# Performance work log

Measured on AMD Instinct MI355X. Metric: run time of the kernel, lower is better.

The kernel has to match this reference:

```python
import jax, jax.numpy as jnp
import numpy as np

B, S, D = 2, 2048, 1024
H, DK = 16, 64
DFF = 4096
WINDOW = 128
GLOBAL = 16
EPS = 1e-5


def _layer_norm(x, g, b):
    mu = jnp.mean(x, axis=-1, keepdims=True)
    var = jnp.var(x, axis=-1, keepdims=True)
    return (x - mu) * jax.lax.rsqrt(var + EPS) * g + b


def setup_inputs() -> dict:
    key = jax.random.key(0)
    ks = jax.random.split(key, 12)
    s = 0.02
    inp = {
        "x": jax.random.normal(ks[0], (B, S, D), dtype=jnp.float32),
        "Wq": jax.random.normal(ks[1], (D, D), jnp.float32) * s,
        "bq": jnp.zeros((D,), jnp.float32),
        "Wk": jax.random.normal(ks[2], (D, D), jnp.float32) * s,
        "bk": jnp.zeros((D,), jnp.float32),
        "Wv": jax.random.normal(ks[3], (D, D), jnp.float32) * s,
        "bv": jnp.zeros((D,), jnp.float32),
        "Wo": jax.random.normal(ks[4], (D, D), jnp.float32) * s,
        "bo": jnp.zeros((D,), jnp.float32),
        "ln1_g": jnp.ones((D,), jnp.float32),
        "ln1_b": jnp.zeros((D,), jnp.float32),
        "W1": jax.random.normal(ks[5], (D, DFF), jnp.float32) * s,
        "b1": jnp.zeros((DFF,), jnp.float32),
        "W2": jax.random.normal(ks[6], (DFF, D), jnp.float32) * s,
        "b2": jnp.zeros((D,), jnp.float32),
        "ln2_g": jnp.ones((D,), jnp.float32),
        "ln2_b": jnp.zeros((D,), jnp.float32),
    }
    return inp


def _local_global_mask(seq_len):
    # token i attends to j iff |i-j| <= WINDOW, or i < GLOBAL, or j < GLOBAL
    i = jnp.arange(seq_len)[:, None]
    j = jnp.arange(seq_len)[None, :]
    m = jnp.abs(i - j) <= WINDOW
    m = m | (i < GLOBAL) | (j < GLOBAL)
    return m  # [S, S] bool


def reference(x, Wq, bq, Wk, bk, Wv, bv, Wo, bo, ln1_g, ln1_b,
              W1, b1, W2, b2, ln2_g, ln2_b):
    # --- self-attention sublayer (pre-norm residual) ---
    xn = _layer_norm(x, ln1_g, ln1_b)
    q = (xn @ Wq + bq).reshape(B, S, H, DK).transpose(0, 2, 1, 3)  # [B,H,S,DK]
    k = (xn @ Wk + bk).reshape(B, S, H, DK).transpose(0, 2, 1, 3)
    v = (xn @ Wv + bv).reshape(B, S, H, DK).transpose(0, 2, 1, 3)

    scores = jnp.einsum('bhqd,bhkd->bhqk', q, k) / jnp.sqrt(jnp.float32(DK))
    mask = _local_global_mask(S)  # [S,S]
    scores = jnp.where(mask[None, None], scores, jnp.float32(-jnp.inf))
    attn = jax.nn.softmax(scores, axis=-1)
    out = jnp.einsum('bhqk,bhkd->bhqd', attn, v)
    out = out.transpose(0, 2, 1, 3).reshape(B, S, D)
    out = out @ Wo + bo
    x = x + out

    # --- feed-forward sublayer (pre-norm residual) ---
    xn2 = _layer_norm(x, ln2_g, ln2_b)
    h = jax.nn.gelu(xn2 @ W1 + b1, approximate=False)
    ff = h @ W2 + b2
    x = x + ff
    return x
```

## Files before the change

### kernel.cpp

```cpp
#include <hip/hip_runtime.h>
#include <stdint.h>


typedef unsigned short u16;
typedef unsigned int   u32;
typedef __attribute__((ext_vector_type(8))) short  short8;
typedef __attribute__((ext_vector_type(4))) float  f32x4;

#define S_LEN   2048
#define D_MODEL 1024
#define ROWS    4096

__device__ __forceinline__ float bf2f(u16 u) {
  union { u32 i; float f; } v; v.i = ((u32)u) << 16; return v.f;
}
__device__ __forceinline__ float bflo(u32 u) {
  union { u32 i; float f; } v; v.i = u << 16; return v.f;
}
__device__ __forceinline__ float bfhi(u32 u) {
  union { u32 i; float f; } v; v.i = u & 0xffff0000u; return v.f;
}
__device__ __forceinline__ u16 f2bf(float f) {
  union { float f; u32 i; } v; v.f = f;
  u32 r = v.i + 0x7fffu + ((v.i >> 16) & 1u);
  return (u16)(r >> 16);
}

__device__ __forceinline__ void gld_lds16(const u16* g, u16* l) {
  __attribute__((address_space(3))) u32* lp =
      reinterpret_cast<__attribute__((address_space(3))) u32*>(
          reinterpret_cast<uintptr_t>(l));
  const __attribute__((address_space(1))) u32* gp =
      reinterpret_cast<const __attribute__((address_space(1))) u32*>(
          reinterpret_cast<uintptr_t>(g));
  __builtin_amdgcn_global_load_lds(gp, lp, 16, 0, 0);
}


#define GBAR  __builtin_amdgcn_s_barrier()
#define LGKM0 asm volatile("s_waitcnt lgkmcnt(0)" ::: "memory")
#define VM4   asm volatile("s_waitcnt vmcnt(4)" ::: "memory")
#define VM0   asm volatile("s_waitcnt vmcnt(0)" ::: "memory")

#define STAGE_A(buf, t, hm) do {                                              \
    gld_lds16(pA[hm][0] + (size_t)(t) * 64, &Ald[buf][0][(hm)*4096 + ldst]);  \
    gld_lds16(pA[hm][1] + (size_t)(t) * 64, &Ald[buf][1][(hm)*4096 + ldst]);  \
  } while (0)

#define STAGE_B(buf, t, hm) do {                                              \
    gld_lds16(pB[hm][0] + (size_t)(t) * 64, &Bld[buf][0][(hm)*4096 + ldst]);  \
    gld_lds16(pB[hm][1] + (size_t)(t) * 64, &Bld[buf][1][(hm)*4096 + ldst]);  \
  } while (0)

#define READ_B(buf) do {                                                      \
    _Pragma("unroll") for (int nj = 0; nj < 4; ++nj) {                        \
      bfv[nj][0] = *(const short8*)&Bld[buf][0][brow + nj * 512];             \
      bfv[nj][1] = *(const short8*)&Bld[buf][1][brow + nj * 512]; }           \
  } while (0)

#define READ_A(buf, q) do {                                                   \
    af[0][0] = *(const short8*)&Ald[buf][0][arow + (2*(q)) * 512];            \
    af[0][1] = *(const short8*)&Ald[buf][1][arow + (2*(q)) * 512];            \
    af[1][0] = *(const short8*)&Ald[buf][0][arow + (2*(q)+1) * 512];          \
    af[1][1] = *(const short8*)&Ald[buf][1][arow + (2*(q)+1) * 512];          \
  } while (0)

#define MFMA_Q(q) do {                                                        \
    __builtin_amdgcn_s_setprio(1);                                            \
    _Pragma("unroll") for (int dm = 0; dm < 2; ++dm)                          \
    _Pragma("unroll") for (int kk = 0; kk < 2; ++kk)                          \
    _Pragma("unroll") for (int nj = 0; nj < 4; ++nj)                          \
      acc[2*(q)+dm][nj] = __builtin_amdgcn_mfma_f32_16x16x32_bf16(            \
          af[dm][kk], bfv[nj][kk], acc[2*(q)+dm][nj], 0, 0, 0);               \
    __builtin_amdgcn_s_setprio(0);                                            \
  } while (0)

#define PHASE(buf, q, STAGE_STMT, TAILWAIT) do {                              \
    if ((q) == 0) READ_B(buf);                                                \
    READ_A(buf, q);                                                           \
    STAGE_STMT;                                                               \
    GBAR;                                                                     \
    LGKM0;                                                                    \
    MFMA_Q(q);                                                                \
    TAILWAIT;                                                                 \
    GBAR;                                                                     \
  } while (0)

template <int EPI>
__global__ __launch_bounds__(512) void gemm256(
    const u16* __restrict__ A, const u16* __restrict__ Bt,
    const float* __restrict__ bias, u16* __restrict__ C,
    int N, int K)
{
  __shared__ __attribute__((aligned(16))) u16 Ald[2][2][256 * 32];
  __shared__ __attribute__((aligned(16))) u16 Bld[2][2][256 * 32];

  const int tid  = threadIdx.x;
  const int w    = tid >> 6;
  const int lane = tid & 63;
  const int wm   = w >> 2;
  const int wn   = w & 3;
  const int lm   = lane & 15;
  const int kq   = lane >> 4;
  const int bm   = blockIdx.y * 256;
  const int bn   = blockIdx.x * 256;

  const int rslot = ((kq + (lm >> 1)) & 3) * 8;
  const int arow  = (wm * 128 + lm) * 32 + rslot;
  const int brow  = (wn * 64  + lm) * 32 + rslot;

  const int gcoff = (((lane & 3) - (lane >> 3)) & 3) * 8;
  const int srow  = w * 16 + (lane >> 2);
  const int ldst  = w * 512;

  const u16* pA[2][2];
  const u16* pB[2][2];
#pragma unroll
  for (int hm = 0; hm < 2; ++hm)
#pragma unroll
    for (int j = 0; j < 2; ++j) {
      pA[hm][j] = A  + (size_t)(bm + hm * 128 + srow) * K + j * 32 + gcoff;
      pB[hm][j] = Bt + (size_t)(bn + hm * 128 + srow) * K + j * 32 + gcoff;
    }

  f32x4 acc[8][4];
#pragma unroll
  for (int i = 0; i < 8; ++i)
#pragma unroll
    for (int j = 0; j < 4; ++j) acc[i][j] = (f32x4){0.f, 0.f, 0.f, 0.f};

  short8 af[2][2];
  short8 bfv[4][2];

  const int P = K >> 7;

  STAGE_B(0, 0, 0); STAGE_B(0, 0, 1);
  STAGE_A(0, 0, 0); STAGE_A(0, 0, 1);
  STAGE_B(1, 1, 0); STAGE_B(1, 1, 1);
  VM4;
  GBAR;

  for (int i = 0; i < P - 1; ++i) {
    const int t1 = 2 * i + 1, t2 = 2 * i + 2, t3 = 2 * i + 3;
    PHASE(0, 0, STAGE_A(1, t1, 0), );
    PHASE(0, 1, STAGE_A(1, t1, 1), );
    PHASE(0, 2, STAGE_B(0, t2, 0), );
    PHASE(0, 3, STAGE_B(0, t2, 1), VM4);
    PHASE(1, 0, STAGE_A(0, t2, 0), );
    PHASE(1, 1, STAGE_A(0, t2, 1), );
    PHASE(1, 2, STAGE_B(1, t3, 0), );
    PHASE(1, 3, STAGE_B(1, t3, 1), VM4);
  }
  {
    const int t1 = 2 * P - 1;
    PHASE(0, 0, STAGE_A(1, t1, 0), );
    PHASE(0, 1, STAGE_A(1, t1, 1), );
    PHASE(0, 2, , );
    PHASE(0, 3, , VM0);
    PHASE(1, 0, , );
    PHASE(1, 1, , );
    PHASE(1, 2, , );
    PHASE(1, 3, , );
  }

  const int r0 = kq * 4;
#pragma unroll
  for (int mi = 0; mi < 8; ++mi) {
#pragma unroll
    for (int r = 0; r < 4; ++r) {
      const int grow = bm + wm * 128 + mi * 16 + r0 + r;
#pragma unroll
      for (int nj = 0; nj < 4; ++nj) {
        const int gcol = bn + wn * 64 + nj * 16 + lm;
        float v = acc[mi][nj][r] + bias[gcol];
        if (EPI == 1) v = 0.5f * v * (1.0f + erff(v * 0.70710678118654752f));
        C[(size_t)grow * N + gcol] = f2bf(v);
      }
    }
  }
}

__global__ __launch_bounds__(256) void gemm_sp(
    const u16* __restrict__ A, const u16* __restrict__ Bt,
    u16* __restrict__ P0, u16* __restrict__ P1,
    int M, int N, int K, int KH)
{
  __shared__ __attribute__((aligned(16))) u16 As[2][128 * 32];
  __shared__ __attribute__((aligned(16))) u16 Bs[2][128 * 32];
  const int tid  = threadIdx.x;
  const int wave = tid >> 6;
  const int lane = tid & 63;
  const int bm = blockIdx.y * 128;
  const int bn = blockIdx.x * 128;
  const int kz = blockIdx.z;
  u16* P = kz ? P1 : P0;
  const int wr = (wave >> 1) * 64;
  const int wc = (wave & 1) * 64;
  const int lm = lane & 15;
  const int kq = lane >> 4;

  f32x4 acc[4][4];
#pragma unroll
  for (int i = 0; i < 4; ++i)
#pragma unroll
    for (int j = 0; j < 4; ++j) acc[i][j] = (f32x4){0.f, 0.f, 0.f, 0.f};

  const int srow = wave * 16 + (lane >> 2);
  const int kg   = (((lane & 3) - (srow >> 1)) & 3) * 8;
  const u16* gA = A  + (size_t)(bm + srow) * K + kz * KH + kg;
  const u16* gB = Bt + (size_t)(bn + srow) * K + kz * KH + kg;
  const int wb = (wave * 16) * 32;

  gld_lds16(gA, &As[0][wb]);
  gld_lds16(gA + (size_t)64 * K, &As[0][wb + 64 * 32]);
  gld_lds16(gB, &Bs[0][wb]);
  gld_lds16(gB + (size_t)64 * K, &Bs[0][wb + 64 * 32]);

  int buf = 0;
  for (int k0 = 0; k0 < KH; k0 += 32, buf ^= 1) {
    __syncthreads();
    const int kn = k0 + 32;
    if (kn < KH) {
      gld_lds16(gA + kn, &As[buf ^ 1][wb]);
      gld_lds16(gA + (size_t)64 * K + kn, &As[buf ^ 1][wb + 64 * 32]);
      gld_lds16(gB + kn, &Bs[buf ^ 1][wb]);
      gld_lds16(gB + (size_t)64 * K + kn, &Bs[buf ^ 1][wb + 64 * 32]);
    }

    short8 af[4], bfv[4];
#pragma unroll
    for (int ti = 0; ti < 4; ++ti) {
      const int Ra = wr + ti * 16 + lm;
      af[ti] = *(const short8*)&As[buf][Ra * 32 + (((kq + (Ra >> 1)) & 3) * 8)];
    }
#pragma unroll
    for (int tj = 0; tj < 4; ++tj) {
      const int Rb = wc + tj * 16 + lm;
      bfv[tj] = *(const short8*)&Bs[buf][Rb * 32 + (((kq + (Rb >> 1)) & 3) * 8)];
    }
#pragma unroll
    for (int ti = 0; ti < 4; ++ti)
#pragma unroll
      for (int tj = 0; tj < 4; ++tj)
        acc[ti][tj] = __builtin_amdgcn_mfma_f32_16x16x32_bf16(
            af[ti], bfv[tj], acc[ti][tj], 0, 0, 0);
  }

  const int r0 = (lane >> 4) * 4;
#pragma unroll
  for (int ti = 0; ti < 4; ++ti) {
#pragma unroll
    for (int r = 0; r < 4; ++r) {
      const int grow = bm + wr + ti * 16 + r0 + r;
#pragma unroll
      for (int tj = 0; tj < 4; ++tj) {
        const int gcol = bn + wc + tj * 16 + lm;
        P[(size_t)grow * N + gcol] = f2bf(acc[ti][tj][r]);
      }
    }
  }
}

__global__ __launch_bounds__(256) void reduce2(
    const u16* __restrict__ P0, const u16* __restrict__ P1,
    const float* __restrict__ bias, const float* res, float* out)
{
  const size_t base = ((size_t)blockIdx.x * 256 + threadIdx.x) * 8;
  const int col = (int)(base & 1023);
  uint4 p0 = *(const uint4*)(P0 + base);
  uint4 p1 = *(const uint4*)(P1 + base);
  float4 b0 = *(const float4*)(bias + col);
  float4 b1 = *(const float4*)(bias + col + 4);
  float4 r0 = *(const float4*)(res + base);
  float4 r1 = *(const float4*)(res + base + 4);
  float4 o0, o1;
  o0.x = bflo(p0.x) + bflo(p1.x) + b0.x + r0.x;
  o0.y = bfhi(p0.x) + bfhi(p1.x) + b0.y + r0.y;
  o0.z = bflo(p0.y) + bflo(p1.y) + b0.z + r0.z;
  o0.w = bfhi(p0.y) + bfhi(p1.y) + b0.w + r0.w;
  o1.x = bflo(p0.z) + bflo(p1.z) + b1.x + r1.x;
  o1.y = bfhi(p0.z) + bfhi(p1.z) + b1.y + r1.y;
  o1.z = bflo(p0.w) + bflo(p1.w) + b1.z + r1.z;
  o1.w = bfhi(p0.w) + bfhi(p1.w) + b1.w + r1.w;
  *(float4*)(out + base) = o0;
  *(float4*)(out + base + 4) = o1;
}

__global__ __launch_bounds__(256) void ln_kernel(
    const float* __restrict__ x, const float* __restrict__ g,
    const float* __restrict__ b, u16* __restrict__ o)
{
  const int row = blockIdx.x;
  const int t = threadIdx.x;
  float4 v = *(const float4*)(x + (size_t)row * D_MODEL + t * 4);
  float s  = v.x + v.y + v.z + v.w;
  float ss = v.x * v.x + v.y * v.y + v.z * v.z + v.w * v.w;
#pragma unroll
  for (int off = 32; off > 0; off >>= 1) {
    s  += __shfl_down(s, off);
    ss += __shfl_down(ss, off);
  }
  __shared__ float sm[4], ssm[4], stat[2];
  if ((t & 63) == 0) { sm[t >> 6] = s; ssm[t >> 6] = ss; }
  __syncthreads();
  if (t == 0) {
    float S = sm[0] + sm[1] + sm[2] + sm[3];
    float SS = ssm[0] + ssm[1] + ssm[2] + ssm[3];
    float mu = S * (1.0f / 1024.0f);
    float var = SS * (1.0f / 1024.0f) - mu * mu;
    stat[0] = mu;
    stat[1] = rsqrtf(fmaxf(var, 0.0f) + 1e-5f);
  }
  __syncthreads();
  const float mu = stat[0], rstd = stat[1];
  float4 gg = *(const float4*)(g + t * 4);
  float4 bb = *(const float4*)(b + t * 4);
  u16 o0 = f2bf((v.x - mu) * rstd * gg.x + bb.x);
  u16 o1 = f2bf((v.y - mu) * rstd * gg.y + bb.y);
  u16 o2 = f2bf((v.z - mu) * rstd * gg.z + bb.z);
  u16 o3 = f2bf((v.w - mu) * rstd * gg.w + bb.w);
  uint2 w;
  w.x = (u32)o0 | ((u32)o1 << 16);
  w.y = (u32)o2 | ((u32)o3 << 16);
  *(uint2*)(o + (size_t)row * D_MODEL + t * 4) = w;
}

__global__ __launch_bounds__(256) void attn_band(
    const u16* __restrict__ qkv, u16* __restrict__ out)
{
  const int t    = threadIdx.x;
  const int w    = t >> 6;
  const int lane = t & 63;
  const int m    = lane & 15;
  const int quad = lane >> 4;
  const int bh   = blockIdx.y;
  const int b    = bh >> 4, h = bh & 15;
  const int i0   = blockIdx.x * 64;
  const size_t bb = (size_t)b * S_LEN;

  __shared__ __attribute__((aligned(16))) u16 Ks[32 * 72];
  __shared__ __attribute__((aligned(16))) u16 Vt[64 * 40];
  __shared__ __attribute__((aligned(16))) u16 Ps[4][16 * 40];

  const u16* qrow = qkv + (bb + i0 + 16 * w + m) * 3072 + h * 64;
  const short8 aq0 = *(const short8*)(qrow + quad * 8);
  const short8 aq1 = *(const short8*)(qrow + 32 + quad * 8);

  f32x4 Ov[4];
#pragma unroll
  for (int td = 0; td < 4; ++td) Ov[td] = (f32x4){0.f, 0.f, 0.f, 0.f};
  float mP[4] = {-1e30f, -1e30f, -1e30f, -1e30f};
  float lS[4] = {0.f, 0.f, 0.f, 0.f};

  const int iB = i0 + 16 * w + quad * 4;

  const int lo = max(32, i0 - 128);
  const int hi = min(S_LEN, i0 + 192);
  const int nChunks = 1 + (hi - lo) / 32;

  const int skr = t >> 3;
  const int skc = (t & 7) * 8;

  for (int c = 0; c < nChunks; ++c) {
    const int j0 = (c == 0) ? 0 : lo + (c - 1) * 32;
    __syncthreads();
    {
      const u16* src = qkv + (bb + j0 + skr) * 3072 + 1024 + h * 64 + skc;
      uint4 kk = *(const uint4*)src;
      uint4 vv = *(const uint4*)(src + 1024);
      *(uint4*)&Ks[skr * 72 + skc] = kk;
      const u16 vs[8] = {
        (u16)(vv.x & 0xffffu), (u16)(vv.x >> 16),
        (u16)(vv.y & 0xffffu), (u16)(vv.y >> 16),
        (u16)(vv.z & 0xffffu), (u16)(vv.z >> 16),
        (u16)(vv.w & 0xffffu), (u16)(vv.w >> 16)};
#pragma unroll
      for (int i = 0; i < 8; ++i) Vt[(skc + i) * 40 + skr] = vs[i];
    }
    __syncthreads();

    const short8 b00 = *(const short8*)&Ks[m * 72 + quad * 8];
    const short8 b01 = *(const short8*)&Ks[m * 72 + 32 + quad * 8];
    const short8 b10 = *(const short8*)&Ks[(16 + m) * 72 + quad * 8];
    const short8 b11 = *(const short8*)&Ks[(16 + m) * 72 + 32 + quad * 8];
    f32x4 s0 = (f32x4){0.f, 0.f, 0.f, 0.f};
    f32x4 s1 = (f32x4){0.f, 0.f, 0.f, 0.f};
    s0 = __builtin_amdgcn_mfma_f32_16x16x32_bf16(aq0, b00, s0, 0, 0, 0);
    s0 = __builtin_amdgcn_mfma_f32_16x16x32_bf16(aq1, b01, s0, 0, 0, 0);
    s1 = __builtin_amdgcn_mfma_f32_16x16x32_bf16(aq0, b10, s1, 0, 0, 0);
    s1 = __builtin_amdgcn_mfma_f32_16x16x32_bf16(aq1, b11, s1, 0, 0, 0);

    const int jA = j0 + m, jB = j0 + 16 + m;
#pragma unroll
    for (int r = 0; r < 4; ++r) {
      const int iG = iB + r;
      const int da = iG - jA, db = iG - jB;
      s0[r] = ((jA < 16) || (da >= -128 && da <= 128)) ? s0[r] * 0.125f : -1e30f;
      s1[r] = ((jB < 16) || (db >= -128 && db <= 128)) ? s1[r] * 0.125f : -1e30f;
    }

    float al[4];
#pragma unroll
    for (int r = 0; r < 4; ++r) {
      float mx = fmaxf(s0[r], s1[r]);
      mx = fmaxf(mx, __shfl_xor(mx, 1, 16));
      mx = fmaxf(mx, __shfl_xor(mx, 2, 16));
      mx = fmaxf(mx, __shfl_xor(mx, 4, 16));
      mx = fmaxf(mx, __shfl_xor(mx, 8, 16));
      const float mn = fmaxf(mP[r], mx);
      al[r] = __expf(mP[r] - mn);
      mP[r] = mn;
      const float p0 = __expf(s0[r] - mn);
      const float p1 = __expf(s1[r] - mn);
      float ps = p0 + p1;
      ps += __shfl_xor(ps, 1, 16);
      ps += __shfl_xor(ps, 2, 16);
      ps += __shfl_xor(ps, 4, 16);
      ps += __shfl_xor(ps, 8, 16);
      lS[r] = lS[r] * al[r] + ps;
      Ps[w][(quad * 4 + r) * 40 + m]      = f2bf(p0);
      Ps[w][(quad * 4 + r) * 40 + 16 + m] = f2bf(p1);
    }
#pragma unroll
    for (int td = 0; td < 4; ++td)
#pragma unroll
      for (int r = 0; r < 4; ++r) Ov[td][r] *= al[r];

    const short8 pa = *(const short8*)&Ps[w][m * 40 + quad * 8];
#pragma unroll
    for (int td = 0; td < 4; ++td) {
      const short8 bv = *(const short8*)&Vt[(td * 16 + m) * 40 + quad * 8];
      Ov[td] = __builtin_amdgcn_mfma_f32_16x16x32_bf16(pa, bv, Ov[td], 0, 0, 0);
    }
  }

  if (i0 + 16 * w >= 16) {
    float inv[4];
#pragma unroll
    for (int r = 0; r < 4; ++r) inv[r] = 1.0f / lS[r];
#pragma unroll
    for (int td = 0; td < 4; ++td)
#pragma unroll
      for (int r = 0; r < 4; ++r)
        out[(bb + iB + r) * 1024 + h * 64 + td * 16 + m] =
            f2bf(Ov[td][r] * inv[r]);
  }
}

__global__ __launch_bounds__(256) void attn_gpart(
    const u16* __restrict__ qkv, float* __restrict__ Obuf,
    float* __restrict__ mbuf, float* __restrict__ lbuf)
{
  const int t    = threadIdx.x;
  const int w    = t >> 6;
  const int lane = t & 63;
  const int m    = lane & 15;
  const int quad = lane >> 4;
  const int kb   = blockIdx.x;
  const int bh   = blockIdx.y;
  const int b    = bh >> 4, h = bh & 15;
  const size_t bb = (size_t)b * S_LEN;

  __shared__ __attribute__((aligned(16))) u16 Ks[4][32 * 72];
  __shared__ __attribute__((aligned(16))) u16 Vt[4][64 * 40];
  __shared__ __attribute__((aligned(16))) u16 Ps[4][16 * 40];

  const u16* qrow = qkv + (bb + m) * 3072 + h * 64;
  const short8 aq0 = *(const short8*)(qrow + quad * 8);
  const short8 aq1 = *(const short8*)(qrow + 32 + quad * 8);

  f32x4 Ov[4];
#pragma unroll
  for (int td = 0; td < 4; ++td) Ov[td] = (f32x4){0.f, 0.f, 0.f, 0.f};
  float mP[4] = {-1e30f, -1e30f, -1e30f, -1e30f};
  float lS[4] = {0.f, 0.f, 0.f, 0.f};

  const int srow = lane >> 1;
  const int sd   = (lane & 1) * 32;

  for (int c = 0; c < 2; ++c) {
    const int j0 = kb * 256 + w * 64 + c * 32;
    {
      const u16* src = qkv + (bb + j0 + srow) * 3072 + 1024 + h * 64 + sd;
      uint4 k0 = *(const uint4*)(src);
      uint4 k1 = *(const uint4*)(src + 8);
      uint4 k2 = *(const uint4*)(src + 16);
      uint4 k3 = *(const uint4*)(src + 24);
      *(uint4*)&Ks[w][srow * 72 + sd]      = k0;
      *(uint4*)&Ks[w][srow * 72 + sd + 8]  = k1;
      *(uint4*)&Ks[w][srow * 72 + sd + 16] = k2;
      *(uint4*)&Ks[w][srow * 72 + sd + 24] = k3;
#pragma unroll
      for (int q4 = 0; q4 < 4; ++q4) {
        uint4 vv = *(const uint4*)(src + 1024 + q4 * 8);
        const u16 vs[8] = {
          (u16)(vv.x & 0xffffu), (u16)(vv.x >> 16),
          (u16)(vv.y & 0xffffu), (u16)(vv.y >> 16),
          (u16)(vv.z & 0xffffu), (u16)(vv.z >> 16),
          (u16)(vv.w & 0xffffu), (u16)(vv.w >> 16)};
#pragma unroll
        for (int i = 0; i < 8; ++i)
          Vt[w][(sd + q4 * 8 + i) * 40 + srow] = vs[i];
      }
    }

    const short8 b00 = *(const short8*)&Ks[w][m * 72 + quad * 8];
    const short8 b01 = *(const short8*)&Ks[w][m * 72 + 32 + quad * 8];
    const short8 b10 = *(const short8*)&Ks[w][(16 + m) * 72 + quad * 8];
    const short8 b11 = *(const short8*)&Ks[w][(16 + m) * 72 + 32 + quad * 8];
    f32x4 s0 = (f32x4){0.f, 0.f, 0.f, 0.f};
    f32x4 s1 = (f32x4){0.f, 0.f, 0.f, 0.f};
    s0 = __builtin_amdgcn_mfma_f32_16x16x32_bf16(aq0, b00, s0, 0, 0, 0);
    s0 = __builtin_amdgcn_mfma_f32_16x16x32_bf16(aq1, b01, s0, 0, 0, 0);
    s1 = __builtin_amdgcn_mfma_f32_16x16x32_bf16(aq0, b10, s1, 0, 0, 0);
    s1 = __builtin_amdgcn_mfma_f32_16x16x32_bf16(aq1, b11, s1, 0, 0, 0);

    float al[4];
#pragma unroll
    for (int r = 0; r < 4; ++r) {
      const float v0 = s0[r] * 0.125f, v1 = s1[r] * 0.125f;
      float mx = fmaxf(v0, v1);
      mx = fmaxf(mx, __shfl_xor(mx, 1, 16));
      mx = fmaxf(mx, __shfl_xor(mx, 2, 16));
      mx = fmaxf(mx, __shfl_xor(mx, 4, 16));
      mx = fmaxf(mx, __shfl_xor(mx, 8, 16));
      const float mn = fmaxf(mP[r], mx);
      al[r] = __expf(mP[r] - mn);
      mP[r] = mn;
      const float p0 = __expf(v0 - mn);
      const float p1 = __expf(v1 - mn);
      float ps = p0 + p1;
      ps += __shfl_xor(ps, 1, 16);
      ps += __shfl_xor(ps, 2, 16);
      ps += __shfl_xor(ps, 4, 16);
      ps += __shfl_xor(ps, 8, 16);
      lS[r] = lS[r] * al[r] + ps;
      Ps[w][(quad * 4 + r) * 40 + m]      = f2bf(p0);
      Ps[w][(quad * 4 + r) * 40 + 16 + m] = f2bf(p1);
    }
#pragma unroll
    for (int td = 0; td < 4; ++td)
#pragma unroll
      for (int r = 0; r < 4; ++r) Ov[td][r] *= al[r];

    const short8 pa = *(const short8*)&Ps[w][m * 40 + quad * 8];
#pragma unroll
    for (int td = 0; td < 4; ++td) {
      const short8 bv = *(const short8*)&Vt[w][(td * 16 + m) * 40 + quad * 8];
      Ov[td] = __builtin_amdgcn_mfma_f32_16x16x32_bf16(pa, bv, Ov[td], 0, 0, 0);
    }
  }

  const int p = kb * 4 + w;
  const size_t ob = ((size_t)(bh * 32 + p)) * 16 * 64;
#pragma unroll
  for (int td = 0; td < 4; ++td)
#pragma unroll
    for (int r = 0; r < 4; ++r)
      Obuf[ob + (size_t)(quad * 4 + r) * 64 + td * 16 + m] = Ov[td][r];
  if (m == 0) {
    const int mb = (bh * 32 + p) * 16;
#pragma unroll
    for (int r = 0; r < 4; ++r) {
      mbuf[mb + quad * 4 + r] = mP[r];
      lbuf[mb + quad * 4 + r] = lS[r];
    }
  }
}

__global__ __launch_bounds__(256) void attn_gcombine(
    const float* __restrict__ Obuf, const float* __restrict__ mbuf,
    const float* __restrict__ lbuf, u16* __restrict__ out)
{
  const int bh = blockIdx.x;
  const int b  = bh >> 4, h = bh & 15;
  const int t  = threadIdx.x;
  const int q  = t >> 4;
  const int d0 = (t & 15) * 4;
  const int mb = bh * 32 * 16;

  float mv[32];
  float M = -1e30f;
#pragma unroll
  for (int p = 0; p < 32; ++p) {
    mv[p] = mbuf[mb + p * 16 + q];
    M = fmaxf(M, mv[p]);
  }
  float L = 0.f;
  float4 acc = {0.f, 0.f, 0.f, 0.f};
#pragma unroll
  for (int p = 0; p < 32; ++p) {
    const float wp = __expf(mv[p] - M);
    L += lbuf[mb + p * 16 + q] * wp;
    float4 o = *(const float4*)&Obuf[(((size_t)(bh * 32 + p)) * 16 + q) * 64 + d0];
    acc.x += wp * o.x; acc.y += wp * o.y;
    acc.z += wp * o.z; acc.w += wp * o.w;
  }
  const float inv = 1.0f / L;
  uint2 wv;
  wv.x = (u32)f2bf(acc.x * inv) | ((u32)f2bf(acc.y * inv) << 16);
  wv.y = (u32)f2bf(acc.z * inv) | ((u32)f2bf(acc.w * inv) << 16);
  *(uint2*)(out + ((size_t)b * S_LEN + q) * 1024 + h * 64 + d0) = wv;
}

__global__ __launch_bounds__(256) void prep_all(
    const float* __restrict__ Wq, const float* __restrict__ Wk,
    const float* __restrict__ Wv, const float* __restrict__ Wo,
    const float* __restrict__ W1, const float* __restrict__ W2,
    const float* __restrict__ bq, const float* __restrict__ bk,
    const float* __restrict__ bv,
    u16* __restrict__ WQKVT, u16* __restrict__ WOT,
    u16* __restrict__ W1T, u16* __restrict__ W2T,
    float* __restrict__ BQKV)
{
  const int gb = blockIdx.x;
  const int t = threadIdx.x;
  if (gb >= 3072) {
    const int i = (gb - 3072) * 256 + t;
    if (i < 1024) BQKV[i] = bq[i];
    else if (i < 2048) BQKV[i] = bk[i - 1024];
    else BQKV[i] = bv[i - 2048];
    return;
  }
  const float* in; u16* outp; int R, Cc, bx, by;
  if (gb < 1024) {
    const int seg = gb >> 8, local = gb & 255;
    bx = local & 15; by = local >> 4; R = 1024; Cc = 1024;
    in   = (seg == 0) ? Wq : (seg == 1) ? Wk : (seg == 2) ? Wv : Wo;
    outp = (seg < 3) ? WQKVT + (size_t)seg * 1024 * 1024 : WOT;
  } else if (gb < 2048) {
    const int local = gb - 1024;
    bx = local & 63; by = local >> 6; R = 1024; Cc = 4096;
    in = W1; outp = W1T;
  } else {
    const int local = gb - 2048;
    bx = local & 15; by = local >> 4; R = 4096; Cc = 1024;
    in = W2; outp = W2T;
  }

  __shared__ u16 tile[64][65];
  const int tr = by * 64, tc = bx * 64;
  const int lr = t >> 2, lc0 = (t & 3) * 16;
  const float* src = in + (size_t)(tr + lr) * Cc + tc + lc0;
  float4 a0 = *(const float4*)(src);
  float4 a1 = *(const float4*)(src + 4);
  float4 a2 = *(const float4*)(src + 8);
  float4 a3 = *(const float4*)(src + 12);
  const float vals[16] = {a0.x, a0.y, a0.z, a0.w, a1.x, a1.y, a1.z, a1.w,
                          a2.x, a2.y, a2.z, a2.w, a3.x, a3.y, a3.z, a3.w};
#pragma unroll
  for (int q = 0; q < 16; ++q) tile[lr][lc0 + q] = f2bf(vals[q]);
  __syncthreads();
  u16* dst = outp + (size_t)(tc + lr) * R + tr + lc0;
  u32 w[8];
#pragma unroll
  for (int q = 0; q < 8; ++q)
    w[q] = (u32)tile[lc0 + 2 * q][lr] | ((u32)tile[lc0 + 2 * q + 1][lr] << 16);
  uint4 s0; s0.x = w[0]; s0.y = w[1]; s0.z = w[2]; s0.w = w[3];
  uint4 s1; s1.x = w[4]; s1.y = w[5]; s1.z = w[6]; s1.w = w[7];
  *(uint4*)dst = s0;
  *(uint4*)(dst + 8) = s1;
}

static const size_t OFF_WQKVT = 0;
static const size_t OFF_WOT   = OFF_WQKVT + (size_t)3072 * 1024 * 2;
static const size_t OFF_W1T   = OFF_WOT   + (size_t)1024 * 1024 * 2;
static const size_t OFF_W2T   = OFF_W1T   + (size_t)4096 * 1024 * 2;
static const size_t OFF_BQKV  = OFF_W2T   + (size_t)1024 * 4096 * 2;
static const size_t OFF_XN    = OFF_BQKV  + 16384;
static const size_t OFF_QKV   = OFF_XN    + (size_t)4096 * 1024 * 2;
static const size_t OFF_AO    = OFF_QKV   + (size_t)4096 * 3072 * 2;
static const size_t OFF_H     = OFF_QKV;

extern "C" void kernel_launch(void* const* d_in, const int* in_sizes, int n_in,
                              void* d_out, int out_size, void* d_ws, size_t ws_size,
                              hipStream_t stream)
{
  const float* x   = (const float*)d_in[0];
  const float* Wq  = (const float*)d_in[1];
  const float* bq  = (const float*)d_in[2];
  const float* Wk  = (const float*)d_in[3];
  const float* bk  = (const float*)d_in[4];
  const float* Wv  = (const float*)d_in[5];
  const float* bv  = (const float*)d_in[6];
  const float* Wo  = (const float*)d_in[7];
  const float* bo  = (const float*)d_in[8];
  const float* g1  = (const float*)d_in[9];
  const float* be1 = (const float*)d_in[10];
  const float* W1  = (const float*)d_in[11];
  const float* b1  = (const float*)d_in[12];
  const float* W2  = (const float*)d_in[13];
  const float* b2  = (const float*)d_in[14];
  const float* g2  = (const float*)d_in[15];
  const float* be2 = (const float*)d_in[16];
  float* outf = (float*)d_out;
  char* ws = (char*)d_ws;

  u16*   WQKVT = (u16*)(ws + OFF_WQKVT);
  u16*   WOT   = (u16*)(ws + OFF_WOT);
  u16*   W1T   = (u16*)(ws + OFF_W1T);
  u16*   W2T   = (u16*)(ws + OFF_W2T);
  float* BQKV  = (float*)(ws + OFF_BQKV);
  u16*   XN    = (u16*)(ws + OFF_XN);
  u16*   QKV   = (u16*)(ws + OFF_QKV);
  u16*   AO    = (u16*)(ws + OFF_AO);
  u16*   Hbuf  = (u16*)(ws + OFF_H);
  float* X1    = outf;
  u16* PWo0 = (u16*)(ws + OFF_QKV);
  u16* PWo1 = PWo0 + (size_t)4096 * 1024;
  u16* PW20 = (u16*)(ws + OFF_W1T);
  u16* PW21 = (u16*)(ws + OFF_XN);
  float* GO = (float*)(ws + OFF_XN);
  float* GM = GO + (size_t)32 * 32 * 16 * 64;
  float* GL = GM + 32 * 32 * 16;

  const dim3 blk(256);
  prep_all<<<dim3(3084), blk, 0, stream>>>(Wq, Wk, Wv, Wo, W1, W2, bq, bk, bv,
                                           WQKVT, WOT, W1T, W2T, BQKV);

  ln_kernel<<<dim3(ROWS), blk, 0, stream>>>(x, g1, be1, XN);
  gemm256<0><<<dim3(12, 16), dim3(512), 0, stream>>>(XN, WQKVT, BQKV, QKV,
                                                     3072, 1024);
  attn_band<<<dim3(32, 32), blk, 0, stream>>>(QKV, AO);
  attn_gpart<<<dim3(8, 32), blk, 0, stream>>>(QKV, GO, GM, GL);
  attn_gcombine<<<dim3(32), blk, 0, stream>>>(GO, GM, GL, AO);
  gemm_sp<<<dim3(8, 32, 2), blk, 0, stream>>>(AO, WOT, PWo0, PWo1,
                                              ROWS, 1024, 1024, 512);
  reduce2<<<dim3(2048), blk, 0, stream>>>(PWo0, PWo1, bo, x, X1);

  ln_kernel<<<dim3(ROWS), blk, 0, stream>>>(X1, g2, be2, XN);
  gemm256<1><<<dim3(16, 16), dim3(512), 0, stream>>>(XN, W1T, b1, Hbuf,
                                                     4096, 1024);
  gemm_sp<<<dim3(8, 32, 2), blk, 0, stream>>>(Hbuf, W2T, PW20, PW21,
                                              ROWS, 1024, 4096, 2048);
  reduce2<<<dim3(2048), blk, 0, stream>>>(PW20, PW21, b2, X1, outf);
}
```

Before: 351.1 us.

## Pipeline LDS fragment reads in gemm256 and use it for split-K projections

```diff
diff --git a/kernel.cpp b/kernel.cpp
--- a/kernel.cpp
+++ b/kernel.cpp
@@ -37,19 +37,18 @@
 }
 
 
-#define GBAR  __builtin_amdgcn_s_barrier()
-#define LGKM0 asm volatile("s_waitcnt lgkmcnt(0)" ::: "memory")
-#define VM4   asm volatile("s_waitcnt vmcnt(4)" ::: "memory")
-#define VM0   asm volatile("s_waitcnt vmcnt(0)" ::: "memory")
+#define GBAR  asm volatile("s_barrier" ::: "memory")
+#define LGKM(n) asm volatile("s_waitcnt lgkmcnt(" #n ")" ::: "memory")
+#define VM(n)   asm volatile("s_waitcnt vmcnt(" #n ")" ::: "memory")
 
 #define STAGE_A(buf, t, hm) do {                                              \
-    gld_lds16(pA[hm][0] + (size_t)(t) * 64, &Ald[buf][0][(hm)*4096 + ldst]);  \
-    gld_lds16(pA[hm][1] + (size_t)(t) * 64, &Ald[buf][1][(hm)*4096 + ldst]);  \
+    gld_lds16(pA##hm + (size_t)(t) * 64,      &Ald[buf][0][(hm)*4096 + ldst]);\
+    gld_lds16(pA##hm + (size_t)(t) * 64 + 32, &Ald[buf][1][(hm)*4096 + ldst]);\
   } while (0)
 
 #define STAGE_B(buf, t, hm) do {                                              \
-    gld_lds16(pB[hm][0] + (size_t)(t) * 64, &Bld[buf][0][(hm)*4096 + ldst]);  \
-    gld_lds16(pB[hm][1] + (size_t)(t) * 64, &Bld[buf][1][(hm)*4096 + ldst]);  \
+    gld_lds16(pB##hm + (size_t)(t) * 64,      &Bld[buf][0][(hm)*4096 + ldst]);\
+    gld_lds16(pB##hm + (size_t)(t) * 64 + 32, &Bld[buf][1][(hm)*4096 + ldst]);\
   } while (0)
 
 #define READ_B(buf) do {                                                      \
@@ -59,10 +58,10 @@
   } while (0)
 
 #define READ_A(buf, q) do {                                                   \
-    af[0][0] = *(const short8*)&Ald[buf][0][arow + (2*(q)) * 512];            \
-    af[0][1] = *(const short8*)&Ald[buf][1][arow + (2*(q)) * 512];            \
-    af[1][0] = *(const short8*)&Ald[buf][0][arow + (2*(q)+1) * 512];          \
-    af[1][1] = *(const short8*)&Ald[buf][1][arow + (2*(q)+1) * 512];          \
+    af[(q)&1][0][0] = *(const short8*)&Ald[buf][0][arow + (2*(q)) * 512];     \
+    af[(q)&1][0][1] = *(const short8*)&Ald[buf][1][arow + (2*(q)) * 512];     \
+    af[(q)&1][1][0] = *(const short8*)&Ald[buf][0][arow + (2*(q)+1) * 512];   \
+    af[(q)&1][1][1] = *(const short8*)&Ald[buf][1][arow + (2*(q)+1) * 512];   \
   } while (0)
 
 #define MFMA_Q(q) do {                                                        \
@@ -71,26 +70,15 @@
     _Pragma("unroll") for (int kk = 0; kk < 2; ++kk)                          \
     _Pragma("unroll") for (int nj = 0; nj < 4; ++nj)                          \
       acc[2*(q)+dm][nj] = __builtin_amdgcn_mfma_f32_16x16x32_bf16(            \
-          af[dm][kk], bfv[nj][kk], acc[2*(q)+dm][nj], 0, 0, 0);               \
+          af[(q)&1][dm][kk], bfv[nj][kk], acc[2*(q)+dm][nj], 0, 0, 0);        \
     __builtin_amdgcn_s_setprio(0);                                            \
   } while (0)
 
-#define PHASE(buf, q, STAGE_STMT, TAILWAIT) do {                              \
-    if ((q) == 0) READ_B(buf);                                                \
-    READ_A(buf, q);                                                           \
-    STAGE_STMT;                                                               \
-    GBAR;                                                                     \
-    LGKM0;                                                                    \
-    MFMA_Q(q);                                                                \
-    TAILWAIT;                                                                 \
-    GBAR;                                                                     \
-  } while (0)
-
-template <int EPI>
+template <int EPI, int KC, int LDK>
 __global__ __launch_bounds__(512) void gemm256(
     const u16* __restrict__ A, const u16* __restrict__ Bt,
-    const float* __restrict__ bias, u16* __restrict__ C,
-    int N, int K)
+    const float* __restrict__ bias, u16* __restrict__ C0,
+    u16* __restrict__ C1, int N)
 {
   __shared__ __attribute__((aligned(16))) u16 Ald[2][2][256 * 32];
   __shared__ __attribute__((aligned(16))) u16 Bld[2][2][256 * 32];
@@ -104,6 +92,11 @@
   const int kq   = lane >> 4;
   const int bm   = blockIdx.y * 256;
   const int bn   = blockIdx.x * 256;
+  const int kz   = blockIdx.z;
+
+  const u16* Ak = A  + (size_t)kz * KC;
+  const u16* Bk = Bt + (size_t)kz * KC;
+  u16* C = kz ? C1 : C0;
 
   const int rslot = ((kq + (lm >> 1)) & 3) * 8;
   const int arow  = (wm * 128 + lm) * 32 + rslot;
@@ -113,15 +106,10 @@
   const int srow  = w * 16 + (lane >> 2);
   const int ldst  = w * 512;
 
-  const u16* pA[2][2];
-  const u16* pB[2][2];
-#pragma unroll
-  for (int hm = 0; hm < 2; ++hm)
-#pragma unroll
-    for (int j = 0; j < 2; ++j) {
-      pA[hm][j] = A  + (size_t)(bm + hm * 128 + srow) * K + j * 32 + gcoff;
-      pB[hm][j] = Bt + (size_t)(bn + hm * 128 + srow) * K + j * 32 + gcoff;
-    }
+  const u16* pA0 = Ak + (size_t)(bm + srow) * LDK + gcoff;
+  const u16* pA1 = pA0 + (size_t)128 * LDK;
+  const u16* pB0 = Bk + (size_t)(bn + srow) * LDK + gcoff;
+  const u16* pB1 = pB0 + (size_t)128 * LDK;
 
   f32x4 acc[8][4];
 #pragma unroll
@@ -129,38 +117,42 @@
 #pragma unroll
     for (int j = 0; j < 4; ++j) acc[i][j] = (f32x4){0.f, 0.f, 0.f, 0.f};
 
-  short8 af[2][2];
+  short8 af[2][2][2];
   short8 bfv[4][2];
 
-  const int P = K >> 7;
+  constexpr int P = KC >> 7;
 
   STAGE_B(0, 0, 0); STAGE_B(0, 0, 1);
   STAGE_A(0, 0, 0); STAGE_A(0, 0, 1);
   STAGE_B(1, 1, 0); STAGE_B(1, 1, 1);
-  VM4;
+  VM(4);
   GBAR;
+  READ_A(0, 0);
 
   for (int i = 0; i < P - 1; ++i) {
     const int t1 = 2 * i + 1, t2 = 2 * i + 2, t3 = 2 * i + 3;
-    PHASE(0, 0, STAGE_A(1, t1, 0), );
-    PHASE(0, 1, STAGE_A(1, t1, 1), );
-    PHASE(0, 2, STAGE_B(0, t2, 0), );
-    PHASE(0, 3, STAGE_B(0, t2, 1), VM4);
-    PHASE(1, 0, STAGE_A(0, t2, 0), );
-    PHASE(1, 1, STAGE_A(0, t2, 1), );
-    PHASE(1, 2, STAGE_B(1, t3, 0), );
-    PHASE(1, 3, STAGE_B(1, t3, 1), VM4);
+    GBAR; STAGE_A(1, t1, 0); READ_B(0); READ_A(0, 1); LGKM(4); MFMA_Q(0);
+    GBAR; STAGE_A(1, t1, 1); READ_A(0, 2);            LGKM(4); MFMA_Q(1);
+    GBAR; STAGE_B(0, t2, 0); READ_A(0, 3);            LGKM(4); MFMA_Q(2);
+    VM(2);
+    GBAR; STAGE_B(0, t2, 1); READ_A(1, 0);            LGKM(4); MFMA_Q(3);
+    GBAR; STAGE_A(0, t2, 0); READ_B(1); READ_A(1, 1); LGKM(4); MFMA_Q(0);
+    GBAR; STAGE_A(0, t2, 1); READ_A(1, 2);            LGKM(4); MFMA_Q(1);
+    GBAR; STAGE_B(1, t3, 0); READ_A(1, 3);            LGKM(4); MFMA_Q(2);
+    VM(2);
+    GBAR; STAGE_B(1, t3, 1); READ_A(0, 0);            LGKM(4); MFMA_Q(3);
   }
   {
     const int t1 = 2 * P - 1;
-    PHASE(0, 0, STAGE_A(1, t1, 0), );
-    PHASE(0, 1, STAGE_A(1, t1, 1), );
-    PHASE(0, 2, , );
-    PHASE(0, 3, , VM0);
-    PHASE(1, 0, , );
-    PHASE(1, 1, , );
-    PHASE(1, 2, , );
-    PHASE(1, 3, , );
+    GBAR; STAGE_A(1, t1, 0); READ_B(0); READ_A(0, 1); LGKM(4); MFMA_Q(0);
+    GBAR; STAGE_A(1, t1, 1); READ_A(0, 2);            LGKM(4); MFMA_Q(1);
+    GBAR;                    READ_A(0, 3);            LGKM(4); MFMA_Q(2);
+    VM(0);
+    GBAR;                    READ_A(1, 0);            LGKM(4); MFMA_Q(3);
+    GBAR;                    READ_B(1); READ_A(1, 1); LGKM(4); MFMA_Q(0);
+    GBAR;                    READ_A(1, 2);            LGKM(4); MFMA_Q(1);
+    GBAR;                    READ_A(1, 3);            LGKM(4); MFMA_Q(2);
+    LGKM(0); MFMA_Q(3);
   }
 
   const int r0 = kq * 4;
@@ -172,90 +164,10 @@
 #pragma unroll
       for (int nj = 0; nj < 4; ++nj) {
         const int gcol = bn + wn * 64 + nj * 16 + lm;
-        float v = acc[mi][nj][r] + bias[gcol];
+        float v = acc[mi][nj][r];
+        if (EPI < 2) v += bias[gcol];
         if (EPI == 1) v = 0.5f * v * (1.0f + erff(v * 0.70710678118654752f));
         C[(size_t)grow * N + gcol] = f2bf(v);
-      }
-    }
-  }
-}
-
-__global__ __launch_bounds__(256) void gemm_sp(
-    const u16* __restrict__ A, const u16* __restrict__ Bt,
-    u16* __restrict__ P0, u16* __restrict__ P1,
-    int M, int N, int K, int KH)
-{
-  __shared__ __attribute__((aligned(16))) u16 As[2][128 * 32];
-  __shared__ __attribute__((aligned(16))) u16 Bs[2][128 * 32];
-  const int tid  = threadIdx.x;
-  const int wave = tid >> 6;
-  const int lane = tid & 63;
-  const int bm = blockIdx.y * 128;
-  const int bn = blockIdx.x * 128;
-  const int kz = blockIdx.z;
-  u16* P = kz ? P1 : P0;
-  const int wr = (wave >> 1) * 64;
-  const int wc = (wave & 1) * 64;
-  const int lm = lane & 15;
-  const int kq = lane >> 4;
-
-  f32x4 acc[4][4];
-#pragma unroll
-  for (int i = 0; i < 4; ++i)
-#pragma unroll
-    for (int j = 0; j < 4; ++j) acc[i][j] = (f32x4){0.f, 0.f, 0.f, 0.f};
-
-  const int srow = wave * 16 + (lane >> 2);
-  const int kg   = (((lane & 3) - (srow >> 1)) & 3) * 8;
-  const u16* gA = A  + (size_t)(bm + srow) * K + kz * KH + kg;
-  const u16* gB = Bt + (size_t)(bn + srow) * K + kz * KH + kg;
-  const int wb = (wave * 16) * 32;
-
-  gld_lds16(gA, &As[0][wb]);
-  gld_lds16(gA + (size_t)64 * K, &As[0][wb + 64 * 32]);
-  gld_lds16(gB, &Bs[0][wb]);
-  gld_lds16(gB + (size_t)64 * K, &Bs[0][wb + 64 * 32]);
-
-  int buf = 0;
-  for (int k0 = 0; k0 < KH; k0 += 32, buf ^= 1) {
-    __syncthreads();
-    const int kn = k0 + 32;
-    if (kn < KH) {
-      gld_lds16(gA + kn, &As[buf ^ 1][wb]);
-      gld_lds16(gA + (size_t)64 * K + kn, &As[buf ^ 1][wb + 64 * 32]);
-      gld_lds16(gB + kn, &Bs[buf ^ 1][wb]);
-      gld_lds16(gB + (size_t)64 * K + kn, &Bs[buf ^ 1][wb + 64 * 32]);
-    }
-
-    short8 af[4], bfv[4];
-#pragma unroll
-    for (int ti = 0; ti < 4; ++ti) {
-      const int Ra = wr + ti * 16 + lm;
-      af[ti] = *(const short8*)&As[buf][Ra * 32 + (((kq + (Ra >> 1)) & 3) * 8)];
-    }
-#pragma unroll
-    for (int tj = 0; tj < 4; ++tj) {
-      const int Rb = wc + tj * 16 + lm;
-      bfv[tj] = *(const short8*)&Bs[buf][Rb * 32 + (((kq + (Rb >> 1)) & 3) * 8)];
-    }
-#pragma unroll
-    for (int ti = 0; ti < 4; ++ti)
-#pragma unroll
-      for (int tj = 0; tj < 4; ++tj)
-        acc[ti][tj] = __builtin_amdgcn_mfma_f32_16x16x32_bf16(
-            af[ti], bfv[tj], acc[ti][tj], 0, 0, 0);
-  }
-
-  const int r0 = (lane >> 4) * 4;
-#pragma unroll
-  for (int ti = 0; ti < 4; ++ti) {
-#pragma unroll
-    for (int r = 0; r < 4; ++r) {
-      const int grow = bm + wr + ti * 16 + r0 + r;
-#pragma unroll
-      for (int tj = 0; tj < 4; ++tj) {
-        const int gcol = bn + wc + tj * 16 + lm;
-        P[(size_t)grow * N + gcol] = f2bf(acc[ti][tj][r]);
       }
     }
   }
@@ -715,23 +627,24 @@
   float* GL = GM + 32 * 32 * 16;
 
   const dim3 blk(256);
+  const dim3 blk512(512);
   prep_all<<<dim3(3084), blk, 0, stream>>>(Wq, Wk, Wv, Wo, W1, W2, bq, bk, bv,
                                            WQKVT, WOT, W1T, W2T, BQKV);
 
   ln_kernel<<<dim3(ROWS), blk, 0, stream>>>(x, g1, be1, XN);
-  gemm256<0><<<dim3(12, 16), dim3(512), 0, stream>>>(XN, WQKVT, BQKV, QKV,
-                                                     3072, 1024);
+  gemm256<0, 1024, 1024><<<dim3(12, 16, 1), blk512, 0, stream>>>(
+      XN, WQKVT, BQKV, QKV, QKV, 3072);
   attn_band<<<dim3(32, 32), blk, 0, stream>>>(QKV, AO);
   attn_gpart<<<dim3(8, 32), blk, 0, stream>>>(QKV, GO, GM, GL);
   attn_gcombine<<<dim3(32), blk, 0, stream>>>(GO, GM, GL, AO);
-  gemm_sp<<<dim3(8, 32, 2), blk, 0, stream>>>(AO, WOT, PWo0, PWo1,
-                                              ROWS, 1024, 1024, 512);
+  gemm256<2, 512, 1024><<<dim3(4, 16, 2), blk512, 0, stream>>>(
+      AO, WOT, nullptr, PWo0, PWo1, 1024);
   reduce2<<<dim3(2048), blk, 0, stream>>>(PWo0, PWo1, bo, x, X1);
 
   ln_kernel<<<dim3(ROWS), blk, 0, stream>>>(X1, g2, be2, XN);
-  gemm256<1><<<dim3(16, 16), dim3(512), 0, stream>>>(XN, W1T, b1, Hbuf,
-                                                     4096, 1024);
-  gemm_sp<<<dim3(8, 32, 2), blk, 0, stream>>>(Hbuf, W2T, PW20, PW21,
-                                              ROWS, 1024, 4096, 2048);
+  gemm256<1, 1024, 1024><<<dim3(16, 16, 1), blk512, 0, stream>>>(
+      XN, W1T, b1, Hbuf, Hbuf, 4096);
+  gemm256<2, 2048, 4096><<<dim3(4, 16, 2), blk512, 0, stream>>>(
+      Hbuf, W2T, nullptr, PW20, PW21, 1024);
   reduce2<<<dim3(2048), blk, 0, stream>>>(PW20, PW21, b2, X1, outf);
 }
```

Result: slower. 358.6 us (+2.1%).
